# Performance work log

Hardware: AMD Instinct MI355X
Metric: run time of the kernel (lower is better)

## Reference

```python
import jax, jax.numpy as jnp
import numpy as np

DIM = 384
HEADS = 12
WS = (7, 7, 7)
N = WS[0] * WS[1] * WS[2]  # 343
NW = 64   # number of windows (mask dim)
B_ = 64   # num_windows * batch
CPB_HIDDEN = 512


def _make_buffers():
    # relative coords table: (1, 2Wd-1, 2Wh-1, 2Ww-1, 3), log-spaced per Swin-V2
    axes = [np.arange(-(w - 1), w, dtype=np.float32) / (w - 1) for w in WS]
    g = np.stack(np.meshgrid(*axes, indexing='ij'), axis=-1)[None]  # (1,13,13,13,3)
    g = g * 8.0
    table = np.sign(g) * np.log2(np.abs(g) + 1.0) / np.log2(8.0)
    # relative position index: (N, N) int
    coords = np.stack(np.meshgrid(*[np.arange(w) for w in WS], indexing='ij'))  # (3,Wd,Wh,Ww)
    cf = coords.reshape(3, -1)
    rel = (cf[:, :, None] - cf[:, None, :]).transpose(1, 2, 0).astype(np.int64)  # (N,N,3)
    rel[..., 0] += WS[0] - 1
    rel[..., 1] += WS[1] - 1
    rel[..., 2] += WS[2] - 1
    rel[..., 0] *= (2 * WS[1] - 1) * (2 * WS[2] - 1)
    rel[..., 1] *= 2 * WS[2] - 1
    idx = rel.sum(-1)
    return jnp.asarray(table, dtype=jnp.float32), jnp.asarray(idx, dtype=jnp.int32)


def setup_inputs() -> dict:
    key = jax.random.key(0)
    ks = jax.random.split(key, 10)
    table, idx = _make_buffers()
    return {
        'x': jax.random.normal(ks[0], (B_, N, DIM), dtype=jnp.float32),
        'mask': jax.random.normal(ks[1], (NW, N, N), dtype=jnp.float32),
        'qkv_w': jax.random.normal(ks[2], (3 * DIM, DIM), dtype=jnp.float32) * 0.02,
        'q_bias': jax.random.normal(ks[3], (DIM,), dtype=jnp.float32) * 0.02,
        'v_bias': jax.random.normal(ks[4], (DIM,), dtype=jnp.float32) * 0.02,
        'logit_scale': jnp.log(10.0 * jnp.ones((HEADS, 1, 1), dtype=jnp.float32)),
        'cpb_w1': jax.random.normal(ks[5], (CPB_HIDDEN, 3), dtype=jnp.float32) * 0.02,
        'cpb_b1': jax.random.normal(ks[6], (CPB_HIDDEN,), dtype=jnp.float32) * 0.02,
        'cpb_w2': jax.random.normal(ks[7], (HEADS, CPB_HIDDEN), dtype=jnp.float32) * 0.02,
        'proj_w': jax.random.normal(ks[8], (DIM, DIM), dtype=jnp.float32) * 0.02,
        'proj_b': jax.random.normal(ks[9], (DIM,), dtype=jnp.float32) * 0.02,
        'rel_table': table,
        'rel_index': idx,
    }


def reference(x, mask, qkv_w, q_bias, v_bias, logit_scale, cpb_w1, cpb_b1,
              cpb_w2, proj_w, proj_b, rel_table, rel_index):
    Bw, n, C = x.shape
    H = logit_scale.shape[0]
    hd = C // H
    qkv_bias = jnp.concatenate([q_bias, jnp.zeros_like(v_bias), v_bias])
    qkv = x @ qkv_w.T + qkv_bias                      # (Bw, n, 3C)
    qkv = qkv.reshape(Bw, n, 3, H, hd).transpose(2, 0, 3, 1, 4)
    q, k, v = qkv[0], qkv[1], qkv[2]                  # (Bw, H, n, hd)
    qn = q / jnp.clip(jnp.linalg.norm(q, axis=-1, keepdims=True), 1e-12)
    kn = k / jnp.clip(jnp.linalg.norm(k, axis=-1, keepdims=True), 1e-12)
    attn = jnp.einsum('bhnd,bhmd->bhnm', qn, kn)
    scale = jnp.exp(jnp.minimum(logit_scale, jnp.log(100.0)))  # clamp max log(1/0.01)
    attn = attn * scale
    # CPB MLP bias: (1,13,13,13,3) -> (table_size, H), gathered to (H, n, n)
    hidden = jax.nn.relu(rel_table @ cpb_w1.T + cpb_b1)
    bias_table = (hidden @ cpb_w2.T).reshape(-1, H)
    bias = bias_table[rel_index.reshape(-1)].reshape(n, n, H).transpose(2, 0, 1)
    bias = 16.0 * jax.nn.sigmoid(bias)
    attn = attn + bias[None]
    nW = mask.shape[0]
    attn = attn.reshape(Bw // nW, nW, H, n, n) + mask[None, :, None]
    attn = attn.reshape(Bw, H, n, n)
    attn = jax.nn.softmax(attn, axis=-1)
    out = jnp.einsum('bhnm,bhmd->bnhd', attn, v).reshape(Bw, n, C)
    out = out @ proj_w.T + proj_b
    return out
```

## Files before the change

kernel.cpp:

```cpp
#include <hip/hip_runtime.h>
#include <hip/hip_bf16.h>
#include <stdint.h>


typedef __attribute__((ext_vector_type(4))) float f32x4;
typedef __attribute__((ext_vector_type(8))) short short8;

#define DIM   384
#define HEADS 12
#define NTOK  343
#define NPAD  352
#define BW    64
#define MROWS (BW*NTOK)
#define MPAD  22016
#define NN    (NTOK*NTOK)
#define BPAD  352
#define LOG2E 1.44269504089f
#define SMAX  48.0f

__device__ __forceinline__ unsigned short f2bf(float f) {
  unsigned u = __float_as_uint(f);
  u += 0x7FFF + ((u >> 16) & 1);
  return (unsigned short)(u >> 16);
}

__device__ __forceinline__ unsigned pk2bf(float lo, float hi) {
  return (__float_as_uint(hi) & 0xFFFF0000u) | (__float_as_uint(lo) >> 16);
}

__device__ __forceinline__ void gload_lds16(const void* g, void* l) {
  __builtin_amdgcn_global_load_lds(
      (const __attribute__((address_space(1))) void*)g,
      (__attribute__((address_space(3))) void*)l, 16, 0, 0);
}

__global__ __launch_bounds__(256) void cvt_bf16(const float* __restrict__ in,
                                                unsigned short* __restrict__ out,
                                                long nvalid, long ntotal) {
  long i = ((long)blockIdx.x * 256 + threadIdx.x) * 8;
  if (i >= ntotal) return;
  short8 o;
  if (i < nvalid) {
    const float4* p = (const float4*)(in + i);
    float4 a = p[0], b = p[1];
    o[0] = (short)f2bf(a.x); o[1] = (short)f2bf(a.y);
    o[2] = (short)f2bf(a.z); o[3] = (short)f2bf(a.w);
    o[4] = (short)f2bf(b.x); o[5] = (short)f2bf(b.y);
    o[6] = (short)f2bf(b.z); o[7] = (short)f2bf(b.w);
  } else {
    o = (short8)0;
  }
  *(short8*)(out + i) = o;
}

__global__ __launch_bounds__(64) void cpb_tab(const float* __restrict__ tbl,
                                              const float* __restrict__ w1,
                                              const float* __restrict__ b1,
                                              const float* __restrict__ w2,
                                              float* __restrict__ btab) {
  const int r = blockIdx.x, lane = threadIdx.x;
  const float t0 = tbl[r*3], t1 = tbl[r*3+1], t2 = tbl[r*3+2];
  float acc[12];
#pragma unroll
  for (int hh = 0; hh < 12; ++hh) acc[hh] = 0.f;
  for (int u = 0; u < 8; ++u) {
    const int j = lane * 8 + u;
    const float hd = fmaxf(w1[j*3]*t0 + w1[j*3+1]*t1 + w1[j*3+2]*t2 + b1[j], 0.f);
#pragma unroll
    for (int hh = 0; hh < 12; ++hh) acc[hh] += hd * w2[hh*512 + j];
  }
#pragma unroll
  for (int hh = 0; hh < 12; ++hh) {
    float v = acc[hh];
    for (int msk = 1; msk < 64; msk <<= 1) v += __shfl_xor(v, msk);
    if (lane == 0) btab[r*12 + hh] = v;
  }
}

__global__ __launch_bounds__(256) void bias_gather(const float* __restrict__ btab,
                                                   const int* __restrict__ ridx,
                                                   float* __restrict__ bfull) {
  const int blk = blockIdx.x;
  const int hh = blk / NTOK, i = blk % NTOK;
  for (int j = threadIdx.x; j < BPAD; j += 256) {
    float o = -1e9f;
    if (j < NTOK) {
      const int idx = ridx[i*NTOK + j];
      const float v = btab[idx*12 + hh];
      o = LOG2E * 16.f / (1.f + __expf(-v)) - SMAX;
    }
    bfull[(size_t)blk*BPAD + j] = o;
  }
}

template<int MODE>
__global__ __launch_bounds__(256, 2) void gemm_k(
    const unsigned short* __restrict__ A, const unsigned short* __restrict__ B,
    unsigned short* __restrict__ o_qn, unsigned short* __restrict__ o_kn,
    unsigned short* __restrict__ o_vT,
    const float* __restrict__ q_bias, const float* __restrict__ v_bias,
    const float* __restrict__ lsc,
    float* __restrict__ o_out, const float* __restrict__ proj_b) {
  __shared__ alignas(16) uint8_t lds[32768];
  const int tid = threadIdx.x, wave = tid >> 6, lane = tid & 63;
  const int row0 = blockIdx.x * 128, col0 = blockIdx.y * 128;
  const int wm = wave & 1, wn = wave >> 1;
  const int l15 = lane & 15, lq = lane >> 4;
  f32x4 acc[4][4];
#pragma unroll
  for (int i = 0; i < 4; ++i)
#pragma unroll
    for (int j = 0; j < 4; ++j) acc[i][j] = (f32x4)0.f;

  const int stg_row = wave * 8 + (lane >> 3);
  const int srcblk = (lane & 7) ^ (lane >> 3);

  for (int kt = 0; kt < 6; ++kt) {
    const int k0 = kt * 64;
#pragma unroll
    for (int c = 0; c < 4; ++c) {
      const int row = c * 32 + stg_row;
      gload_lds16(A + (size_t)(row0 + row) * DIM + k0 + srcblk * 8,
                  lds + c * 4096 + wave * 1024);
      gload_lds16(B + (size_t)(col0 + row) * DIM + k0 + srcblk * 8,
                  lds + 16384 + c * 4096 + wave * 1024);
    }
    __syncthreads();
#pragma unroll
    for (int s = 0; s < 2; ++s) {
      short8 af[4], bfr[4];
#pragma unroll
      for (int i = 0; i < 4; ++i) {
        const int r = wm * 64 + i * 16 + l15;
        af[i] = *(const short8*)(lds + r * 128 + (((s * 4) | lq) ^ (r & 7)) * 16);
        const int cc = wn * 64 + i * 16 + l15;
        bfr[i] = *(const short8*)(lds + 16384 + cc * 128 + (((s * 4) | lq) ^ (cc & 7)) * 16);
      }
#pragma unroll
      for (int i = 0; i < 4; ++i)
#pragma unroll
        for (int j = 0; j < 4; ++j)
          acc[i][j] = __builtin_amdgcn_mfma_f32_16x16x32_bf16(af[i], bfr[j], acc[i][j], 0, 0, 0);
    }
    __syncthreads();
  }

  if (MODE == 0) {
#pragma unroll
    for (int i = 0; i < 4; ++i) {
      const int gr0 = row0 + wm * 64 + i * 16 + lq * 4;
#pragma unroll
      for (int p = 0; p < 2; ++p) {
        f32x4 c0 = acc[i][2 * p], c1 = acc[i][2 * p + 1];
        const int gcb = col0 + wn * 64 + p * 32;
        const int which = gcb / DIM, rem = gcb % DIM, hh = rem / 32;
        float b0 = 0.f, b1 = 0.f;
        if (which == 0) { b0 = q_bias[rem + l15]; b1 = q_bias[rem + l15 + 16]; }
        else if (which == 2) { b0 = v_bias[rem + l15]; b1 = v_bias[rem + l15 + 16]; }
#pragma unroll
        for (int r = 0; r < 4; ++r) { c0[r] += b0; c1[r] += b1; }
        float mult[4] = {1.f, 1.f, 1.f, 1.f};
        if (which < 2) {
          f32x4 ss;
#pragma unroll
          for (int r = 0; r < 4; ++r) ss[r] = c0[r] * c0[r] + c1[r] * c1[r];
#pragma unroll
          for (int msk = 1; msk < 16; msk <<= 1) {
#pragma unroll
            for (int r = 0; r < 4; ++r) ss[r] += __shfl_xor(ss[r], msk);
          }
          float sc = 1.f;
          if (which == 0)
            sc = __expf(fminf(lsc[hh], 4.6051701860f)) * LOG2E;
#pragma unroll
          for (int r = 0; r < 4; ++r) mult[r] = sc / fmaxf(sqrtf(ss[r]), 1e-12f);
        }
#pragma unroll
        for (int r = 0; r < 4; ++r) {
          const int gr = gr0 + r;
          if (gr >= MROWS) continue;
          const int b = gr / NTOK, nt = gr % NTOK;
          const unsigned short v0 = f2bf(c0[r] * mult[r]);
          const unsigned short v1 = f2bf(c1[r] * mult[r]);
          if (which == 0) {
            const size_t base = ((size_t)(b * HEADS + hh) * NTOK + nt) * 32 + l15;
            o_qn[base] = v0; o_qn[base + 16] = v1;
          } else if (which == 1) {
            const size_t base = ((size_t)(b * HEADS + hh) * NTOK + nt) * 32 + l15;
            o_kn[base] = v0; o_kn[base + 16] = v1;
          } else {
            const size_t base = ((size_t)(b * HEADS + hh) * 32 + l15) * NPAD + nt;
            o_vT[base] = v0; o_vT[base + (size_t)16 * NPAD] = v1;
          }
        }
      }
    }
  } else {
#pragma unroll
    for (int i = 0; i < 4; ++i) {
      const int gr0 = row0 + wm * 64 + i * 16 + lq * 4;
#pragma unroll
      for (int j = 0; j < 4; ++j) {
        const int gc = col0 + wn * 64 + j * 16 + l15;
        const float pb = proj_b[gc];
#pragma unroll
        for (int r = 0; r < 4; ++r) {
          const int gr = gr0 + r;
          if (gr < MROWS) o_out[(size_t)gr * DIM + gc] = acc[i][j][r] + pb;
        }
      }
    }
  }
}

__global__ __launch_bounds__(256, 4) void attn_k(
    const unsigned short* __restrict__ qn, const unsigned short* __restrict__ kn,
    const unsigned short* __restrict__ vT, const float* __restrict__ bfull,
    const float* __restrict__ mask, unsigned short* __restrict__ out1) {
  __shared__ alignas(16) uint8_t lds[38400];
  const int g = blockIdx.x;
  const int idx = g >> 3;
  const int b = (g & 7) * 8 + idx / 24;
  const int r24 = idx % 24;
  const int hh = r24 >> 1, half = r24 & 1;
  const int bh = b * HEADS + hh;
  const int tid = threadIdx.x;

  for (int r = tid; r < NPAD; r += 256) {
    uint4* dst = (uint4*)(lds + r * 80);
    if (r < NTOK) {
      const uint4* src = (const uint4*)(kn + ((size_t)bh * NTOK + r) * 32);
      dst[0] = src[0]; dst[1] = src[1]; dst[2] = src[2]; dst[3] = src[3];
    } else {
      uint4 z = make_uint4(0, 0, 0, 0);
      dst[0] = z; dst[1] = z; dst[2] = z; dst[3] = z;
    }
  }
  __syncthreads();

  const int wave = tid >> 6, lane = tid & 63;
  const int l15 = lane & 15, lq = lane >> 4;
  uint8_t* pb0 = lds + 28160 + wave * 2560;
  uint8_t* pb1 = pb0 + 1280;

  const unsigned short* vrow0 = vT + ((size_t)bh * 32 + l15) * NPAD;
  const unsigned short* vrow1 = vT + ((size_t)bh * 32 + 16 + l15) * NPAD;

  for (int t = wave; t < 11; t += 4) {
    const int q0 = (half * 11 + t) * 16;
    const int qc = min(q0 + l15, NTOK - 1);
    const short8 aq = *(const short8*)(qn + ((size_t)bh * NTOK + qc) * 32 + lq * 8);
    const float* brow = bfull + ((size_t)hh * NTOK + qc) * BPAD;
    const float* mrow = mask + (size_t)b * NN + (size_t)qc * NTOK;

    f32x4 o0 = (f32x4)0.f, o1 = (f32x4)0.f;
    float l_run = 0.f;

    f32x4 pbA[2], pbB[2];
    float pmA[2][4], pmB[2][4];
    short8 kf0[2], kf1[2], vf0[2], vf1[2];

    pbA[0] = *(const f32x4*)(brow + lq * 4);
    pbB[0] = *(const f32x4*)(brow + 16 + lq * 4);
#pragma unroll
    for (int r = 0; r < 4; ++r) {
      pmA[0][r] = mrow[lq * 4 + r];
      pmB[0][r] = mrow[16 + lq * 4 + r];
    }
    kf0[0] = *(const short8*)(lds + l15 * 80 + lq * 16);
    kf1[0] = *(const short8*)(lds + (16 + l15) * 80 + lq * 16);

#pragma unroll
    for (int c = 0; c <= 10; ++c) {
      const int cur = c & 1, nxt = cur ^ 1;
      const int kc = c * 32;
      vf0[cur] = *(const short8*)(vrow0 + kc + lq * 8);
      vf1[cur] = *(const short8*)(vrow1 + kc + lq * 8);
      if (c < 10) {
        const int k2 = kc + 32;
        pbA[nxt] = *(const f32x4*)(brow + k2 + lq * 4);
        pbB[nxt] = *(const f32x4*)(brow + k2 + 16 + lq * 4);
#pragma unroll
        for (int r = 0; r < 4; ++r) {
          pmA[nxt][r] = mrow[k2 + lq * 4 + r];
          const int kk = k2 + 16 + lq * 4 + r;
          pmB[nxt][r] = mrow[(c == 9 && kk >= NTOK) ? 0 : kk];
        }
        kf0[nxt] = *(const short8*)(lds + (k2 + l15) * 80 + lq * 16);
        kf1[nxt] = *(const short8*)(lds + (k2 + 16 + l15) * 80 + lq * 16);
      }
      f32x4 s0 = __builtin_amdgcn_mfma_f32_16x16x32_bf16(kf0[cur], aq, (f32x4)0.f, 0, 0, 0);
      f32x4 s1 = __builtin_amdgcn_mfma_f32_16x16x32_bf16(kf1[cur], aq, (f32x4)0.f, 0, 0, 0);
      float p0[4], p1[4], ps = 0.f;
#pragma unroll
      for (int r = 0; r < 4; ++r) {
        p0[r] = exp2f(s0[r] + fmaf(pmA[cur][r], LOG2E, pbA[cur][r]));
        p1[r] = exp2f(s1[r] + fmaf(pmB[cur][r], LOG2E, pbB[cur][r]));
        ps += p0[r] + p1[r];
      }
      l_run += ps;
      uint8_t* pw = (cur ? pb1 : pb0) + l15 * 80;
      *(uint2*)(pw + lq * 8)      = make_uint2(pk2bf(p0[0], p0[1]), pk2bf(p0[2], p0[3]));
      *(uint2*)(pw + 32 + lq * 8) = make_uint2(pk2bf(p1[0], p1[1]), pk2bf(p1[2], p1[3]));
      if (c > 0) {
        const short8 pf = *(const short8*)((nxt ? pb1 : pb0) + l15 * 80 + lq * 16);
        o0 = __builtin_amdgcn_mfma_f32_16x16x32_bf16(pf, vf0[nxt], o0, 0, 0, 0);
        o1 = __builtin_amdgcn_mfma_f32_16x16x32_bf16(pf, vf1[nxt], o1, 0, 0, 0);
      }
    }
    {
      const short8 pf = *(const short8*)(pb0 + l15 * 80 + lq * 16);
      o0 = __builtin_amdgcn_mfma_f32_16x16x32_bf16(pf, vf0[0], o0, 0, 0, 0);
      o1 = __builtin_amdgcn_mfma_f32_16x16x32_bf16(pf, vf1[0], o1, 0, 0, 0);
    }
    l_run += __shfl_xor(l_run, 16);
    l_run += __shfl_xor(l_run, 32);
    const float invl = 1.f / l_run;
    float ir[4];
#pragma unroll
    for (int r = 0; r < 4; ++r) ir[r] = __shfl(invl, lq * 4 + r);
#pragma unroll
    for (int r = 0; r < 4; ++r) {
      const int q = q0 + lq * 4 + r;
      if (q < NTOK) {
        const size_t base = ((size_t)b * NTOK + q) * DIM + hh * 32 + l15;
        out1[base]      = f2bf(o0[r] * ir[r]);
        out1[base + 16] = f2bf(o1[r] * ir[r]);
      }
    }
  }
}

extern "C" void kernel_launch(void* const* d_in, const int* in_sizes, int n_in,
                              void* d_out, int out_size, void* d_ws, size_t ws_size,
                              hipStream_t stream) {
  const float* x      = (const float*)d_in[0];
  const float* mask   = (const float*)d_in[1];
  const float* qkv_w  = (const float*)d_in[2];
  const float* q_bias = (const float*)d_in[3];
  const float* v_bias = (const float*)d_in[4];
  const float* lsc    = (const float*)d_in[5];
  const float* cpb_w1 = (const float*)d_in[6];
  const float* cpb_b1 = (const float*)d_in[7];
  const float* cpb_w2 = (const float*)d_in[8];
  const float* proj_w = (const float*)d_in[9];
  const float* proj_b = (const float*)d_in[10];
  const float* rtab   = (const float*)d_in[11];
  const int*   ridx   = (const int*)d_in[12];
  float* out = (float*)d_out;
  uint8_t* ws = (uint8_t*)d_ws;

  size_t o = 0;
  auto alloc = [&](size_t bytes) { size_t r = o; o += (bytes + 255) & ~(size_t)255; return r; };
  const size_t off_xb  = alloc((size_t)MPAD * DIM * 2);
  const size_t off_qwb = alloc((size_t)1152 * DIM * 2);
  const size_t off_pwb = alloc((size_t)DIM * DIM * 2);
  const size_t off_qnb = alloc((size_t)BW * HEADS * NTOK * 32 * 2);
  const size_t off_knb = alloc((size_t)BW * HEADS * NTOK * 32 * 2);
  const size_t off_vTb = alloc((size_t)BW * HEADS * 32 * NPAD * 2);
  const size_t off_btab  = alloc((size_t)2197 * 12 * 4);
  const size_t off_bfull = alloc((size_t)HEADS * NTOK * BPAD * 4);
  (void)in_sizes; (void)n_in; (void)out_size;

  if (ws_size < o) {
    hipMemsetAsync(d_out, 0, (size_t)out_size * 4, stream);
    return;
  }

  unsigned short* xb  = (unsigned short*)(ws + off_xb);
  unsigned short* o1b = xb;
  unsigned short* qwb = (unsigned short*)(ws + off_qwb);
  unsigned short* pwb = (unsigned short*)(ws + off_pwb);
  unsigned short* qnb = (unsigned short*)(ws + off_qnb);
  unsigned short* knb = (unsigned short*)(ws + off_knb);
  unsigned short* vTb = (unsigned short*)(ws + off_vTb);
  float* btab  = (float*)(ws + off_btab);
  float* bfull = (float*)(ws + off_bfull);

  cvt_bf16<<<(long)MPAD * DIM / 8 / 256, 256, 0, stream>>>(x, xb, (long)MROWS * DIM, (long)MPAD * DIM);
  cvt_bf16<<<1152 * DIM / 8 / 256, 256, 0, stream>>>(qkv_w, qwb, 1152L * DIM, 1152L * DIM);
  cvt_bf16<<<DIM * DIM / 8 / 256, 256, 0, stream>>>(proj_w, pwb, (long)DIM * DIM, (long)DIM * DIM);
  cpb_tab<<<2197, 64, 0, stream>>>(rtab, cpb_w1, cpb_b1, cpb_w2, btab);
  bias_gather<<<HEADS * NTOK, 256, 0, stream>>>(btab, ridx, bfull);
  gemm_k<0><<<dim3(MPAD / 128, 1152 / 128), 256, 0, stream>>>(
      xb, qwb, qnb, knb, vTb, q_bias, v_bias, lsc, nullptr, nullptr);
  attn_k<<<2 * BW * HEADS, 256, 0, stream>>>(qnb, knb, vTb, bfull, mask, o1b);
  gemm_k<1><<<dim3(MPAD / 128, DIM / 128), 256, 0, stream>>>(
      o1b, pwb, nullptr, nullptr, nullptr, nullptr, nullptr, nullptr, out, proj_b);
}
```

Measured before the change: 356.0 us.

## Merge attention query halves per block and deepen bias/mask prefetch

Each attention block now handles all 22 query tiles of one (batch, head) instead of splitting them across two blocks, so K is staged into LDS once per head rather than twice. The bias and mask loads are prefetched two chunks ahead, V fragments one chunk ahead, and the P reload from LDS is issued before the score MFMAs to hide latency. V rows are interleaved so each lane writes its two output columns as one packed 32-bit store. The trade-offs are half as many blocks (less parallelism), more live registers (launch bounds lowered to 3 blocks per CU), and an output column permutation that only works if the vT layout is consistent with it.

```diff
diff --git a/kernel.cpp b/kernel.cpp
--- a/kernel.cpp
+++ b/kernel.cpp
@@ -213,16 +213,14 @@
   }
 }
 
-__global__ __launch_bounds__(256, 4) void attn_k(
+__global__ __launch_bounds__(256, 3) void attn_k(
     const unsigned short* __restrict__ qn, const unsigned short* __restrict__ kn,
     const unsigned short* __restrict__ vT, const float* __restrict__ bfull,
     const float* __restrict__ mask, unsigned short* __restrict__ out1) {
   __shared__ alignas(16) uint8_t lds[38400];
   const int g = blockIdx.x;
-  const int idx = g >> 3;
-  const int b = (g & 7) * 8 + idx / 24;
-  const int r24 = idx % 24;
-  const int hh = r24 >> 1, half = r24 & 1;
+  const int b = (g & 7) * 8 + (g >> 3) / HEADS;
+  const int hh = (g >> 3) % HEADS;
   const int bh = b * HEADS + hh;
   const int tid = threadIdx.x;
 
@@ -243,11 +241,11 @@
   uint8_t* pb0 = lds + 28160 + wave * 2560;
   uint8_t* pb1 = pb0 + 1280;
 
-  const unsigned short* vrow0 = vT + ((size_t)bh * 32 + l15) * NPAD;
-  const unsigned short* vrow1 = vT + ((size_t)bh * 32 + 16 + l15) * NPAD;
-
-  for (int t = wave; t < 11; t += 4) {
-    const int q0 = (half * 11 + t) * 16;
+  const unsigned short* vrow0 = vT + ((size_t)bh * 32 + 2 * l15) * NPAD;
+  const unsigned short* vrow1 = vT + ((size_t)bh * 32 + 2 * l15 + 1) * NPAD;
+
+  for (int t = wave; t < 22; t += 4) {
+    const int q0 = t * 16;
     const int qc = min(q0 + l15, NTOK - 1);
     const short8 aq = *(const short8*)(qn + ((size_t)bh * NTOK + qc) * 32 + lq * 8);
     const float* brow = bfull + ((size_t)hh * NTOK + qc) * BPAD;
@@ -262,40 +260,55 @@
 
     pbA[0] = *(const f32x4*)(brow + lq * 4);
     pbB[0] = *(const f32x4*)(brow + 16 + lq * 4);
+    pbA[1] = *(const f32x4*)(brow + 32 + lq * 4);
+    pbB[1] = *(const f32x4*)(brow + 48 + lq * 4);
 #pragma unroll
     for (int r = 0; r < 4; ++r) {
       pmA[0][r] = mrow[lq * 4 + r];
       pmB[0][r] = mrow[16 + lq * 4 + r];
+      pmA[1][r] = mrow[32 + lq * 4 + r];
+      pmB[1][r] = mrow[48 + lq * 4 + r];
     }
     kf0[0] = *(const short8*)(lds + l15 * 80 + lq * 16);
     kf1[0] = *(const short8*)(lds + (16 + l15) * 80 + lq * 16);
+    vf0[0] = *(const short8*)(vrow0 + lq * 8);
+    vf1[0] = *(const short8*)(vrow1 + lq * 8);
 
 #pragma unroll
     for (int c = 0; c <= 10; ++c) {
       const int cur = c & 1, nxt = cur ^ 1;
-      const int kc = c * 32;
-      vf0[cur] = *(const short8*)(vrow0 + kc + lq * 8);
-      vf1[cur] = *(const short8*)(vrow1 + kc + lq * 8);
-      if (c < 10) {
-        const int k2 = kc + 32;
-        pbA[nxt] = *(const f32x4*)(brow + k2 + lq * 4);
-        pbB[nxt] = *(const f32x4*)(brow + k2 + 16 + lq * 4);
+      const f32x4 cBA = pbA[cur], cBB = pbB[cur];
+      float cMA[4], cMB[4];
+#pragma unroll
+      for (int r = 0; r < 4; ++r) { cMA[r] = pmA[cur][r]; cMB[r] = pmB[cur][r]; }
+      const short8 vA = vf0[nxt], vB = vf1[nxt];
+      if (c <= 8) {
+        const int k2 = (c + 2) * 32;
+        pbA[cur] = *(const f32x4*)(brow + k2 + lq * 4);
+        pbB[cur] = *(const f32x4*)(brow + k2 + 16 + lq * 4);
 #pragma unroll
         for (int r = 0; r < 4; ++r) {
-          pmA[nxt][r] = mrow[k2 + lq * 4 + r];
+          pmA[cur][r] = mrow[k2 + lq * 4 + r];
           const int kk = k2 + 16 + lq * 4 + r;
-          pmB[nxt][r] = mrow[(c == 9 && kk >= NTOK) ? 0 : kk];
+          pmB[cur][r] = mrow[(c == 8 && kk >= NTOK) ? 0 : kk];
         }
-        kf0[nxt] = *(const short8*)(lds + (k2 + l15) * 80 + lq * 16);
-        kf1[nxt] = *(const short8*)(lds + (k2 + 16 + l15) * 80 + lq * 16);
-      }
+      }
+      if (c <= 9) {
+        const int k1 = (c + 1) * 32;
+        vf0[nxt] = *(const short8*)(vrow0 + k1 + lq * 8);
+        vf1[nxt] = *(const short8*)(vrow1 + k1 + lq * 8);
+        kf0[nxt] = *(const short8*)(lds + (k1 + l15) * 80 + lq * 16);
+        kf1[nxt] = *(const short8*)(lds + (k1 + 16 + l15) * 80 + lq * 16);
+      }
+      short8 pf;
+      if (c > 0) pf = *(const short8*)((nxt ? pb1 : pb0) + l15 * 80 + lq * 16);
       f32x4 s0 = __builtin_amdgcn_mfma_f32_16x16x32_bf16(kf0[cur], aq, (f32x4)0.f, 0, 0, 0);
       f32x4 s1 = __builtin_amdgcn_mfma_f32_16x16x32_bf16(kf1[cur], aq, (f32x4)0.f, 0, 0, 0);
       float p0[4], p1[4], ps = 0.f;
 #pragma unroll
       for (int r = 0; r < 4; ++r) {
-        p0[r] = exp2f(s0[r] + fmaf(pmA[cur][r], LOG2E, pbA[cur][r]));
-        p1[r] = exp2f(s1[r] + fmaf(pmB[cur][r], LOG2E, pbB[cur][r]));
+        p0[r] = exp2f(s0[r] + fmaf(cMA[r], LOG2E, cBA[r]));
+        p1[r] = exp2f(s1[r] + fmaf(cMB[r], LOG2E, cBB[r]));
         ps += p0[r] + p1[r];
       }
       l_run += ps;
@@ -303,9 +316,8 @@
       *(uint2*)(pw + lq * 8)      = make_uint2(pk2bf(p0[0], p0[1]), pk2bf(p0[2], p0[3]));
       *(uint2*)(pw + 32 + lq * 8) = make_uint2(pk2bf(p1[0], p1[1]), pk2bf(p1[2], p1[3]));
       if (c > 0) {
-        const short8 pf = *(const short8*)((nxt ? pb1 : pb0) + l15 * 80 + lq * 16);
-        o0 = __builtin_amdgcn_mfma_f32_16x16x32_bf16(pf, vf0[nxt], o0, 0, 0, 0);
-        o1 = __builtin_amdgcn_mfma_f32_16x16x32_bf16(pf, vf1[nxt], o1, 0, 0, 0);
+        o0 = __builtin_amdgcn_mfma_f32_16x16x32_bf16(pf, vA, o0, 0, 0, 0);
+        o1 = __builtin_amdgcn_mfma_f32_16x16x32_bf16(pf, vB, o1, 0, 0, 0);
       }
     }
     {
@@ -323,9 +335,9 @@
     for (int r = 0; r < 4; ++r) {
       const int q = q0 + lq * 4 + r;
       if (q < NTOK) {
-        const size_t base = ((size_t)b * NTOK + q) * DIM + hh * 32 + l15;
-        out1[base]      = f2bf(o0[r] * ir[r]);
-        out1[base + 16] = f2bf(o1[r] * ir[r]);
+        const size_t base = ((size_t)b * NTOK + q) * DIM + hh * 32 + 2 * l15;
+        *(unsigned*)(out1 + base) =
+            (((unsigned)f2bf(o1[r] * ir[r])) << 16) | f2bf(o0[r] * ir[r]);
       }
     }
   }
@@ -384,7 +396,7 @@
   bias_gather<<<HEADS * NTOK, 256, 0, stream>>>(btab, ridx, bfull);
   gemm_k<0><<<dim3(MPAD / 128, 1152 / 128), 256, 0, stream>>>(
       xb, qwb, qnb, knb, vTb, q_bias, v_bias, lsc, nullptr, nullptr);
-  attn_k<<<2 * BW * HEADS, 256, 0, stream>>>(qnb, knb, vTb, bfull, mask, o1b);
+  attn_k<<<BW * HEADS, 256, 0, stream>>>(qnb, knb, vTb, bfull, mask, o1b);
   gemm_k<1><<<dim3(MPAD / 128, DIM / 128), 256, 0, stream>>>(
       o1b, pwb, nullptr, nullptr, nullptr, nullptr, nullptr, nullptr, out, proj_b);
 }
```

Result: faster. 322.8 us (-9.3%).
